# Optimization experiments

Hardware: AMD Instinct MI355X
Metric: run time of the kernel (lower is better)

## Reference

```python
import jax, jax.numpy as jnp
import numpy as np

H = 16      # num_heads
EPS = 1e-6  # LayerNorm eps


def _ln(x, g, b):
    m = jnp.mean(x, -1, keepdims=True)
    v = jnp.mean((x - m) ** 2, -1, keepdims=True)
    return (x - m) / jnp.sqrt(v + EPS) * g + b


def _mha(q_in, k_in, v_in, qw, qb, kw, kb, vw, vb, pw, pb, mask):
    # q_in: (B, Sq, C); k_in/v_in: (B, Skv, C); mask: bool (Sq, Skv) or None (True = masked)
    B, Sq, C = q_in.shape
    hd = C // H

    def split(x, w, bb):
        return (x @ w + bb).reshape(B, -1, H, hd).transpose(0, 2, 1, 3)  # (B,H,S,hd)

    q = split(q_in, qw, qb) * hd ** -0.5
    k = split(k_in, kw, kb)
    v = split(v_in, vw, vb)
    s = jnp.einsum('bhqd,bhkd->bhqk', q, k)  # (B,H,Sq,Skv)
    if mask is not None:
        s = jnp.where(mask, -jnp.inf, s)
    a = jax.nn.softmax(s, axis=-1)
    o = jnp.einsum('bhqk,bhkd->bhqd', a, v)
    return o.transpose(0, 2, 1, 3).reshape(B, Sq, C) @ pw + pb


def _mlp(x, w1, b1, w2, b2):
    # torch nn.GELU default is exact (erf) gelu
    return jax.nn.gelu(x @ w1 + b1, approximate=False) @ w2 + b2


def setup_inputs() -> dict:
    key = jax.random.key(0)
    B, S, C, M = 1, 2048, 1024, 4096
    ks = iter(jax.random.split(key, 64))

    def w(shape):
        return jax.random.normal(next(ks), shape, jnp.float32) * 0.02

    inp = {
        'features': jax.random.normal(next(ks), (B, S, C), jnp.float32),
        'encoder_output': jax.random.normal(next(ks), (B, S, C), jnp.float32),
    }
    for p in ['ln1a', 'ln1b', 'ln2a', 'ln2b']:
        inp[p + '_g'] = jnp.ones((C,), jnp.float32)
        inp[p + '_b'] = jnp.zeros((C,), jnp.float32)
    for p in ['sa', 'ca']:
        for q in ['q', 'k', 'v', 'p']:
            inp[f'{p}_{q}w'] = w((C, C))
            inp[f'{p}_{q}b'] = jnp.zeros((C,), jnp.float32)
    for p in ['m1', 'm2']:
        inp[p + '_w1'] = w((C, M))
        inp[p + '_b1'] = jnp.zeros((M,), jnp.float32)
        inp[p + '_w2'] = w((M, C))
        inp[p + '_b2'] = jnp.zeros((C,), jnp.float32)
    return inp


def reference(features, encoder_output,
              ln1a_g, ln1a_b, ln1b_g, ln1b_b, ln2a_g, ln2a_b, ln2b_g, ln2b_b,
              sa_qw, sa_qb, sa_kw, sa_kb, sa_vw, sa_vb, sa_pw, sa_pb,
              ca_qw, ca_qb, ca_kw, ca_kb, ca_vw, ca_vb, ca_pw, ca_pb,
              m1_w1, m1_b1, m1_w2, m1_b2, m2_w1, m2_b1, m2_w2, m2_b2):
    S = features.shape[1]
    causal = jnp.triu(jnp.ones((S, S), dtype=bool), 1)  # look-ahead mask (decoder)
    # self-attention block (pre-norm, residual; dropout/drop-path identity in eval)
    xn = _ln(features, ln1a_g, ln1a_b)
    x = features + _mha(xn, xn, xn, sa_qw, sa_qb, sa_kw, sa_kb, sa_vw, sa_vb, sa_pw, sa_pb, causal)
    x = x + _mlp(_ln(x, ln1b_g, ln1b_b), m1_w1, m1_b1, m1_w2, m1_b2)
    # cross-attention block: k = v = encoder_output, q = norm(x)
    xn = _ln(x, ln2a_g, ln2a_b)
    x = x + _mha(xn, encoder_output, encoder_output, ca_qw, ca_qb, ca_kw, ca_kb, ca_vw, ca_vb, ca_pw, ca_pb, None)
    return x + _mlp(_ln(x, ln2b_g, ln2b_b), m2_w1, m2_b1, m2_w2, m2_b2)
```

## Files before the change

### kernel.cpp

```cpp
#include <hip/hip_runtime.h>
#include <math.h>

typedef unsigned short u16;
typedef __bf16 bf16_t;
typedef bf16_t bf16x8 __attribute__((ext_vector_type(8)));
typedef float f32x4 __attribute__((ext_vector_type(4)));
typedef float f32x16 __attribute__((ext_vector_type(16)));

#define DI __device__ __forceinline__

DI u16 f2bf(float f) {
  union { float f; unsigned u; } c; c.f = f;
  unsigned r = c.u + 0x7FFFu + ((c.u >> 16) & 1u);
  return (u16)(r >> 16);
}

DI unsigned pack2(float lo, float hi_) {
  return (unsigned)f2bf(lo) | ((unsigned)f2bf(hi_) << 16);
}

typedef __attribute__((address_space(1))) void* gas_ptr;
typedef __attribute__((address_space(3))) void* las_ptr;

DI void gload16(const void* g, void* l) {
  __builtin_amdgcn_global_load_lds((gas_ptr)g, (las_ptr)l, 16, 0, 0);
}

struct TransArgs { const float* src[12]; u16* dst[12]; };
__global__ __launch_bounds__(256) void k_transpose_all(TransArgs ta) {
  __shared__ float tile[32][33];
  int bx = blockIdx.x;
  int z, local, K, N;
  if (bx < 8192) { z = bx >> 10; local = bx & 1023; K = 1024; N = 1024; }
  else {
    int i = bx - 8192; z = 8 + (i >> 12); local = i & 4095;
    if (z & 1) { K = 4096; N = 1024; } else { K = 1024; N = 4096; }
  }
  const float* w = ta.src[z];
  u16* wt = ta.dst[z];
  int nT = N >> 5;
  int n0 = (local % nT) * 32, k0 = (local / nT) * 32;
  int tx = threadIdx.x & 31, ty = threadIdx.x >> 5;
  for (int r = ty; r < 32; r += 8)
    tile[r][tx] = w[(size_t)(k0 + r) * N + n0 + tx];
  __syncthreads();
  for (int r = ty; r < 32; r += 8)
    wt[(size_t)(n0 + r) * K + k0 + tx] = f2bf(tile[tx][r]);
}

__global__ __launch_bounds__(256) void k_cvt(const float* __restrict__ in, u16* __restrict__ out, int n4) {
  int i = blockIdx.x * 256 + threadIdx.x;
  if (i < n4) {
    float4 v = ((const float4*)in)[i];
    ushort4 o;
    o.x = f2bf(v.x); o.y = f2bf(v.y); o.z = f2bf(v.z); o.w = f2bf(v.w);
    ((ushort4*)out)[i] = o;
  }
}

__global__ __launch_bounds__(256) void k_biaspack(float* __restrict__ bq, float* __restrict__ bc,
                                                  const float* qb, const float* kb, const float* vb,
                                                  const float* ckb, const float* cvb) {
  int i = blockIdx.x * 256 + threadIdx.x;
  if (i < 1024) bq[i] = qb[i];
  else if (i < 2048) bq[i] = kb[i - 1024];
  else if (i < 3072) bq[i] = vb[i - 2048];
  else if (i < 4096) bc[i - 3072] = ckb[i - 3072];
  else if (i < 5120) bc[i - 3072] = cvb[i - 4096];
}

__global__ __launch_bounds__(256) void k_ln(const float* __restrict__ x, const float* __restrict__ g,
                                            const float* __restrict__ b, u16* __restrict__ out) {
  int row = blockIdx.x, t = threadIdx.x;
  const float4 v = ((const float4*)(x + (size_t)row * 1024))[t];
  float s = v.x + v.y + v.z + v.w;
  float ss = v.x * v.x + v.y * v.y + v.z * v.z + v.w * v.w;
  for (int o = 32; o; o >>= 1) { s += __shfl_down(s, o); ss += __shfl_down(ss, o); }
  __shared__ float red[10];
  int w = t >> 6;
  if ((t & 63) == 0) { red[w] = s; red[4 + w] = ss; }
  __syncthreads();
  if (t == 0) {
    float S = red[0] + red[1] + red[2] + red[3];
    float SS = red[4] + red[5] + red[6] + red[7];
    float mean = S * (1.f / 1024.f);
    float var = SS * (1.f / 1024.f) - mean * mean;
    red[8] = mean; red[9] = rsqrtf(var + 1e-6f);
  }
  __syncthreads();
  float mean = red[8], rstd = red[9];
  float4 gg = ((const float4*)g)[t], bb = ((const float4*)b)[t];
  ushort4 o4;
  o4.x = f2bf((v.x - mean) * rstd * gg.x + bb.x);
  o4.y = f2bf((v.y - mean) * rstd * gg.y + bb.y);
  o4.z = f2bf((v.z - mean) * rstd * gg.z + bb.z);
  o4.w = f2bf((v.w - mean) * rstd * gg.w + bb.w);
  ((ushort4*)(out + (size_t)row * 1024))[t] = o4;
}

template <int MODE>
__global__ __launch_bounds__(256) void k_gemm(const u16* __restrict__ A, const u16* __restrict__ Bt,
                                              const float* __restrict__ bias, void* outv, u16* vtout,
                                              int M, int N, int K, int ostride,
                                              float scale, int scale_end, int vcol0) {
  constexpr int BM = 64, NT = 2;
  __shared__ u16 aL[2][BM * 64];
  __shared__ u16 bL[2][128 * 64];
  const int lane = threadIdx.x & 63, w = threadIdx.x >> 6, t = threadIdx.x;
  const int wn = w;
  const int m0 = blockIdx.y * BM, n0 = blockIdx.x * 128;

  f32x4 acc[4][NT];
#pragma unroll
  for (int i = 0; i < 4; ++i)
#pragma unroll
    for (int j = 0; j < NT; ++j) acc[i][j] = (f32x4){0.f, 0.f, 0.f, 0.f};

  auto stage = [&](int buf, int kt) {
    const int k0 = kt << 6;
#pragma unroll
    for (int c = t; c < BM * 8; c += 256) {
      int row = c >> 3, c16 = c & 7;
      int sw = (c16 * 16) ^ ((row & 7) << 4);
      gload16((const char*)(A + (size_t)(m0 + row) * K + k0) + sw, (char*)aL[buf] + c * 16);
    }
#pragma unroll
    for (int c = t; c < 1024; c += 256) {
      int row = c >> 3, c16 = c & 7;
      int sw = (c16 * 16) ^ ((row & 7) << 4);
      gload16((const char*)(Bt + (size_t)(n0 + row) * K + k0) + sw, (char*)bL[buf] + c * 16);
    }
  };

  const int nkt = K >> 6;
  stage(0, 0);
  __syncthreads();
  int cur = 0;
  for (int kt = 0; kt < nkt; ++kt) {
    if (kt + 1 < nkt) stage(cur ^ 1, kt + 1);
#pragma unroll
    for (int kk = 0; kk < 2; ++kk) {
      const int cb = kk * 64 + ((lane >> 4) << 4);
      bf16x8 af[4], bfr[NT];
#pragma unroll
      for (int mi = 0; mi < 4; ++mi) {
        int row = mi * 16 + (lane & 15);
        af[mi] = *(const bf16x8*)((const char*)aL[cur] + row * 128 + (cb ^ ((row & 7) << 4)));
      }
#pragma unroll
      for (int ni = 0; ni < NT; ++ni) {
        int row = wn * 32 + ni * 16 + (lane & 15);
        bfr[ni] = *(const bf16x8*)((const char*)bL[cur] + row * 128 + (cb ^ ((row & 7) << 4)));
      }
#pragma unroll
      for (int mi = 0; mi < 4; ++mi)
#pragma unroll
        for (int ni = 0; ni < NT; ++ni)
          acc[mi][ni] = __builtin_amdgcn_mfma_f32_16x16x32_bf16(af[mi], bfr[ni], acc[mi][ni], 0, 0, 0);
    }
    __syncthreads();
    cur ^= 1;
  }

  const int cBase = n0 + wn * 32 + (lane & 15);
  const int rBase = m0 + ((lane >> 4) << 2);
#pragma unroll
  for (int ni = 0; ni < NT; ++ni) {
    int col = cBase + ni * 16;
    float bv = bias[col];
#pragma unroll
    for (int mi = 0; mi < 4; ++mi) {
      int row = rBase + mi * 16;
      f32x4 a = acc[mi][ni];
      if (MODE == 0) {
        float sc = (col < scale_end) ? scale : 1.f;
        if (col >= vcol0) {
          ushort4 o4;
          o4.x = f2bf((a[0] + bv) * sc); o4.y = f2bf((a[1] + bv) * sc);
          o4.z = f2bf((a[2] + bv) * sc); o4.w = f2bf((a[3] + bv) * sc);
          *(ushort4*)(vtout + (size_t)(col - vcol0) * M + row) = o4;
        } else {
#pragma unroll
          for (int r = 0; r < 4; ++r)
            ((u16*)outv)[(size_t)(row + r) * ostride + col] = f2bf((a[r] + bv) * sc);
        }
      } else {
#pragma unroll
        for (int r = 0; r < 4; ++r) {
          float v = a[r] + bv;
          ((u16*)outv)[(size_t)(row + r) * ostride + col] =
              f2bf(0.5f * v * (1.f + erff(v * 0.70710678118654752f)));
        }
      }
    }
  }
}

template <int MODE>
__global__ __launch_bounds__(512, 2) void k_gemm_sk(const u16* __restrict__ A, const u16* __restrict__ Bt,
                                                    const float* __restrict__ bias, const float* res,
                                                    void* outv, int M, int N, int K, float scale) {
  __shared__ u16 aL[2][2][64 * 64];
  __shared__ u16 bL[2][2][64 * 64];
  const int t = threadIdx.x, lane = t & 63, w = t >> 6;
  const int kh = w >> 2, ws2 = w & 3;
  const int ts = t & 255;
  const int m0 = blockIdx.y * 64, n0 = blockIdx.x * 64;
  const int nktH = (K >> 6) >> 1;
  const int kbase = kh * nktH;

  f32x4 acc[4];
#pragma unroll
  for (int i = 0; i < 4; ++i) acc[i] = (f32x4){0.f, 0.f, 0.f, 0.f};

  auto stage = [&](int buf, int kt) {
    const int k0 = (kbase + kt) << 6;
#pragma unroll
    for (int i = 0; i < 2; ++i) {
      int c = i * 256 + ts;
      int row = c >> 3, c16 = c & 7;
      int sw = (c16 * 16) ^ ((row & 7) << 4);
      gload16((const char*)(A + (size_t)(m0 + row) * K + k0) + sw, (char*)aL[kh][buf] + c * 16);
      gload16((const char*)(Bt + (size_t)(n0 + row) * K + k0) + sw, (char*)bL[kh][buf] + c * 16);
    }
  };

  stage(0, 0);
  __syncthreads();
  int cur = 0;
  for (int kt = 0; kt < nktH; ++kt) {
    if (kt + 1 < nktH) stage(cur ^ 1, kt + 1);
#pragma unroll
    for (int kk = 0; kk < 2; ++kk) {
      const int cb = kk * 64 + ((lane >> 4) << 4);
      bf16x8 af[4], bfr;
#pragma unroll
      for (int mi = 0; mi < 4; ++mi) {
        int row = mi * 16 + (lane & 15);
        af[mi] = *(const bf16x8*)((const char*)aL[kh][cur] + row * 128 + (cb ^ ((row & 7) << 4)));
      }
      {
        int row = ws2 * 16 + (lane & 15);
        bfr = *(const bf16x8*)((const char*)bL[kh][cur] + row * 128 + (cb ^ ((row & 7) << 4)));
      }
#pragma unroll
      for (int mi = 0; mi < 4; ++mi)
        acc[mi] = __builtin_amdgcn_mfma_f32_16x16x32_bf16(af[mi], bfr, acc[mi], 0, 0, 0);
    }
    __syncthreads();
    cur ^= 1;
  }

  float* mergeF = (float*)aL;
  const int r0l = (lane >> 4) << 2, col16 = lane & 15;
  if (kh == 1) {
#pragma unroll
    for (int mi = 0; mi < 4; ++mi)
#pragma unroll
      for (int r = 0; r < 4; ++r)
        mergeF[(ws2 * 64 + mi * 16 + r0l + r) * 17 + col16] = acc[mi][r];
  }
  __syncthreads();
  if (kh == 0) {
    int col = n0 + ws2 * 16 + col16;
    float bv = bias[col];
#pragma unroll
    for (int mi = 0; mi < 4; ++mi) {
      int row = m0 + mi * 16 + r0l;
#pragma unroll
      for (int r = 0; r < 4; ++r) {
        float v = acc[mi][r] + mergeF[(ws2 * 64 + mi * 16 + r0l + r) * 17 + col16] + bv;
        size_t idx = (size_t)(row + r) * N + col;
        if (MODE == 0) ((u16*)outv)[idx] = f2bf(v * scale);
        else ((float*)outv)[idx] = res[idx] + v;
      }
    }
  }
}

template <bool CAUSAL>
__global__ __launch_bounds__(512, 2) void k_attn3(const u16* __restrict__ Q, const u16* __restrict__ K,
                                                  const u16* __restrict__ VT, u16* __restrict__ O,
                                                  int S, int qstride, int kstride) {
  __shared__ __align__(16) char smem[64 * 1024 + 2048 + 8192];
  const int t = threadIdx.x, lane = t & 63, w = t >> 6;
  const int ks = w & 3, qw = w >> 2;
  const int lo5 = lane & 31, hi = lane >> 5;
  const int h = blockIdx.x;
  const int bq = blockIdx.y;
  const int qt = (bq & 1) ? (31 - (bq >> 1)) : (bq >> 1);
  const int hd0 = h * 64;
  const int q0 = qt * 64 + qw * 32;
  const int ts = qw * 64 + lane;

  u16* kL = (u16*)(smem + ks * 16384);
  u16* vL = (u16*)(smem + ks * 16384 + 8192);

  bf16x8 qf[4];
#pragma unroll
  for (int sl = 0; sl < 4; ++sl)
    qf[sl] = *(const bf16x8*)(Q + (size_t)(q0 + lo5) * qstride + hd0 + sl * 16 + hi * 8);

  f32x16 oa0 = {}, oa1 = {};
  float mrun = -1e30f, lsum = 0.f;

  const int nkt = CAUSAL ? (qt + 1) : (S >> 6);
  const int nIter = (nkt + 3) >> 2;

  for (int i = 0; i < nIter; ++i) {
    const int kt = ks + 4 * i;
    const bool active = kt < nkt;
    if (active) {
#pragma unroll
      for (int j = 0; j < 4; ++j) {
        int c = j * 128 + ts, row = c >> 3, c16 = c & 7;
        int sw = (c16 * 16) ^ ((row & 7) << 4);
        gload16((const char*)(K + (size_t)(kt * 64 + row) * kstride + hd0) + sw, (char*)kL + c * 16);
      }
#pragma unroll
      for (int j = 0; j < 4; ++j) {
        int c = j * 128 + ts, row = c >> 3, c16 = c & 7;
        int sw = (c16 * 16) ^ ((row & 7) << 4);
        gload16((const char*)(VT + (size_t)(hd0 + row) * S + kt * 64) + sw, (char*)vL + c * 16);
      }
    }
    __syncthreads();
    if (active) {
      f32x16 s0 = {}, s1 = {};
#pragma unroll
      for (int sl = 0; sl < 4; ++sl) {
        int cb = sl * 32 + hi * 16;
        int r0 = lo5, r1 = 32 + lo5;
        bf16x8 kf0 = *(const bf16x8*)((const char*)kL + r0 * 128 + (cb ^ ((r0 & 7) << 4)));
        bf16x8 kf1 = *(const bf16x8*)((const char*)kL + r1 * 128 + (cb ^ ((r1 & 7) << 4)));
        s0 = __builtin_amdgcn_mfma_f32_32x32x16_bf16(kf0, qf[sl], s0, 0, 0, 0);
        s1 = __builtin_amdgcn_mfma_f32_32x32x16_bf16(kf1, qf[sl], s1, 0, 0, 0);
      }

      if (CAUSAL && kt == qt) {
        int qg = q0 + lo5;
#pragma unroll
        for (int r = 0; r < 16; ++r) {
          int kg = kt * 64 + (r & 3) + 8 * (r >> 2) + 4 * hi;
          if (kg > qg) s0[r] = -1e30f;
          if (kg + 32 > qg) s1[r] = -1e30f;
        }
      }

      float pm = s0[0];
#pragma unroll
      for (int r = 1; r < 16; ++r) pm = fmaxf(pm, s0[r]);
#pragma unroll
      for (int r = 0; r < 16; ++r) pm = fmaxf(pm, s1[r]);
      pm = fmaxf(pm, __shfl_xor(pm, 32));

      float mnew = fmaxf(mrun, pm);
      float sc = exp2f(mrun - mnew);
      lsum *= sc;
#pragma unroll
      for (int r = 0; r < 16; ++r) { oa0[r] *= sc; oa1[r] *= sc; }
      mrun = mnew;

      float ps = 0.f;
#pragma unroll
      for (int r = 0; r < 16; ++r) { s0[r] = exp2f(s0[r] - mrun); ps += s0[r]; }
#pragma unroll
      for (int r = 0; r < 16; ++r) { s1[r] = exp2f(s1[r] - mrun); ps += s1[r]; }
      ps += __shfl_xor(ps, 32);
      lsum += ps;

#pragma unroll
      for (int ksl = 0; ksl < 4; ++ksl) {
        const int base = 8 * (ksl & 1);
        float pA0, pA1, pA2, pA3, pB0, pB1, pB2, pB3;
        if (ksl < 2) {
          pA0 = s0[base + 0]; pA1 = s0[base + 1]; pA2 = s0[base + 2]; pA3 = s0[base + 3];
          pB0 = s0[base + 4]; pB1 = s0[base + 5]; pB2 = s0[base + 6]; pB3 = s0[base + 7];
        } else {
          pA0 = s1[base + 0]; pA1 = s1[base + 1]; pA2 = s1[base + 2]; pA3 = s1[base + 3];
          pB0 = s1[base + 4]; pB1 = s1[base + 5]; pB2 = s1[base + 6]; pB3 = s1[base + 7];
        }
        unsigned a01 = pack2(pA0, pA1), a23 = pack2(pA2, pA3);
        unsigned b01 = pack2(pB0, pB1), b23 = pack2(pB2, pB3);
        unsigned xa01 = __shfl_xor(a01, 32), xa23 = __shfl_xor(a23, 32);
        unsigned xb01 = __shfl_xor(b01, 32), xb23 = __shfl_xor(b23, 32);
        union { unsigned u[4]; bf16x8 v; } pf;
        pf.u[0] = hi ? xb01 : a01;
        pf.u[1] = hi ? xb23 : a23;
        pf.u[2] = hi ? b01 : xa01;
        pf.u[3] = hi ? b23 : xa23;
        int cb = ksl * 32 + hi * 16;
        int r0 = lo5, r1 = 32 + lo5;
        bf16x8 vf0 = *(const bf16x8*)((const char*)vL + r0 * 128 + (cb ^ ((r0 & 7) << 4)));
        bf16x8 vf1 = *(const bf16x8*)((const char*)vL + r1 * 128 + (cb ^ ((r1 & 7) << 4)));
        oa0 = __builtin_amdgcn_mfma_f32_32x32x16_bf16(vf0, pf.v, oa0, 0, 0, 0);
        oa1 = __builtin_amdgcn_mfma_f32_32x32x16_bf16(vf1, pf.v, oa1, 0, 0, 0);
      }
    }
    __syncthreads();
  }

  float* mlBuf = (float*)(smem + 65536);
#define OB_BYTE(g, halfoff) (lo5 * 256 + (((halfoff) + 32 * (g) + 16 * hi) ^ ((lo5 & 15) << 4)))
  if (ks >= 2) {
    char* ob = smem + (qw * 2 + (ks - 2)) * 8192;
#pragma unroll
    for (int g = 0; g < 4; ++g) {
      *(float4*)(ob + OB_BYTE(g, 0)) = make_float4(oa0[4 * g + 0], oa0[4 * g + 1], oa0[4 * g + 2], oa0[4 * g + 3]);
      *(float4*)(ob + OB_BYTE(g, 128)) = make_float4(oa1[4 * g + 0], oa1[4 * g + 1], oa1[4 * g + 2], oa1[4 * g + 3]);
    }
    if (hi == 0) { mlBuf[(w * 32 + lo5) * 2] = mrun; mlBuf[(w * 32 + lo5) * 2 + 1] = lsum; }
  }
  __syncthreads();
  if (ks < 2) {
    int pw = qw * 4 + ks + 2;
    char* ob = smem + (qw * 2 + ks) * 8192;
    float mB = mlBuf[(pw * 32 + lo5) * 2], lB = mlBuf[(pw * 32 + lo5) * 2 + 1];
    float M = fmaxf(mrun, mB);
    float sA = exp2f(mrun - M), sB = exp2f(mB - M);
    lsum = lsum * sA + lB * sB;
    mrun = M;
#pragma unroll
    for (int g = 0; g < 4; ++g) {
      float4 v0 = *(const float4*)(ob + OB_BYTE(g, 0));
      float4 v1 = *(const float4*)(ob + OB_BYTE(g, 128));
      oa0[4 * g + 0] = oa0[4 * g + 0] * sA + v0.x * sB;
      oa0[4 * g + 1] = oa0[4 * g + 1] * sA + v0.y * sB;
      oa0[4 * g + 2] = oa0[4 * g + 2] * sA + v0.z * sB;
      oa0[4 * g + 3] = oa0[4 * g + 3] * sA + v0.w * sB;
      oa1[4 * g + 0] = oa1[4 * g + 0] * sA + v1.x * sB;
      oa1[4 * g + 1] = oa1[4 * g + 1] * sA + v1.y * sB;
      oa1[4 * g + 2] = oa1[4 * g + 2] * sA + v1.z * sB;
      oa1[4 * g + 3] = oa1[4 * g + 3] * sA + v1.w * sB;
    }
  }
  if (ks == 1) {
    char* ob = smem + 32768 + qw * 8192;
#pragma unroll
    for (int g = 0; g < 4; ++g) {
      *(float4*)(ob + OB_BYTE(g, 0)) = make_float4(oa0[4 * g + 0], oa0[4 * g + 1], oa0[4 * g + 2], oa0[4 * g + 3]);
      *(float4*)(ob + OB_BYTE(g, 128)) = make_float4(oa1[4 * g + 0], oa1[4 * g + 1], oa1[4 * g + 2], oa1[4 * g + 3]);
    }
    if (hi == 0) { mlBuf[(w * 32 + lo5) * 2] = mrun; mlBuf[(w * 32 + lo5) * 2 + 1] = lsum; }
  }
  __syncthreads();
  if (ks == 0) {
    int pw = qw * 4 + 1;
    char* ob = smem + 32768 + qw * 8192;
    float mB = mlBuf[(pw * 32 + lo5) * 2], lB = mlBuf[(pw * 32 + lo5) * 2 + 1];
    float M = fmaxf(mrun, mB);
    float sA = exp2f(mrun - M), sB = exp2f(mB - M);
    lsum = lsum * sA + lB * sB;
#pragma unroll
    for (int g = 0; g < 4; ++g) {
      float4 v0 = *(const float4*)(ob + OB_BYTE(g, 0));
      float4 v1 = *(const float4*)(ob + OB_BYTE(g, 128));
      oa0[4 * g + 0] = oa0[4 * g + 0] * sA + v0.x * sB;
      oa0[4 * g + 1] = oa0[4 * g + 1] * sA + v0.y * sB;
      oa0[4 * g + 2] = oa0[4 * g + 2] * sA + v0.z * sB;
      oa0[4 * g + 3] = oa0[4 * g + 3] * sA + v0.w * sB;
      oa1[4 * g + 0] = oa1[4 * g + 0] * sA + v1.x * sB;
      oa1[4 * g + 1] = oa1[4 * g + 1] * sA + v1.y * sB;
      oa1[4 * g + 2] = oa1[4 * g + 2] * sA + v1.z * sB;
      oa1[4 * g + 3] = oa1[4 * g + 3] * sA + v1.w * sB;
    }
    float inv = 1.f / lsum;
    u16* ldsO = (u16*)(smem + 65536 + 2048);
    int qrow = qw * 32 + lo5;
#pragma unroll
    for (int g = 0; g < 4; ++g) {
      unsigned w0 = pack2(oa0[4 * g + 0] * inv, oa0[4 * g + 1] * inv);
      unsigned w1 = pack2(oa0[4 * g + 2] * inv, oa0[4 * g + 3] * inv);
      int dby = (8 * g + 4 * hi) * 2;
      *(uint2*)((char*)ldsO + qrow * 128 + (dby ^ ((qrow & 7) << 4))) = make_uint2(w0, w1);
      unsigned w2 = pack2(oa1[4 * g + 0] * inv, oa1[4 * g + 1] * inv);
      unsigned w3 = pack2(oa1[4 * g + 2] * inv, oa1[4 * g + 3] * inv);
      int dby2 = (32 + 8 * g + 4 * hi) * 2;
      *(uint2*)((char*)ldsO + qrow * 128 + (dby2 ^ ((qrow & 7) << 4))) = make_uint2(w2, w3);
    }
  }
  __syncthreads();
  {
    u16* ldsO = (u16*)(smem + 65536 + 2048);
    int c = t, row = c >> 3, c16 = c & 7;
    uint4 val = *(const uint4*)((const char*)ldsO + row * 128 + ((c16 * 16) ^ ((row & 7) << 4)));
    *(uint4*)(O + (size_t)(qt * 64 + row) * 1024 + hd0 + c16 * 8) = val;
  }
#undef OB_BYTE
}

extern "C" void kernel_launch(void* const* d_in, const int* in_sizes, int n_in,
                              void* d_out, int out_size, void* d_ws, size_t ws_size,
                              hipStream_t stream) {
  const float* features = (const float*)d_in[0];
  const float* enc      = (const float*)d_in[1];
  const float* g1a = (const float*)d_in[2];  const float* b1a = (const float*)d_in[3];
  const float* g1b = (const float*)d_in[4];  const float* b1b = (const float*)d_in[5];
  const float* g2a = (const float*)d_in[6];  const float* b2a = (const float*)d_in[7];
  const float* g2b = (const float*)d_in[8];  const float* b2b = (const float*)d_in[9];
  const float* sa_qw = (const float*)d_in[10]; const float* sa_qb = (const float*)d_in[11];
  const float* sa_kw = (const float*)d_in[12]; const float* sa_kb = (const float*)d_in[13];
  const float* sa_vw = (const float*)d_in[14]; const float* sa_vb = (const float*)d_in[15];
  const float* sa_pw = (const float*)d_in[16]; const float* sa_pb = (const float*)d_in[17];
  const float* ca_qw = (const float*)d_in[18]; const float* ca_qb = (const float*)d_in[19];
  const float* ca_kw = (const float*)d_in[20]; const float* ca_kb = (const float*)d_in[21];
  const float* ca_vw = (const float*)d_in[22]; const float* ca_vb = (const float*)d_in[23];
  const float* ca_pw = (const float*)d_in[24]; const float* ca_pb = (const float*)d_in[25];
  const float* m1_w1 = (const float*)d_in[26]; const float* m1_b1 = (const float*)d_in[27];
  const float* m1_w2 = (const float*)d_in[28]; const float* m1_b2 = (const float*)d_in[29];
  const float* m2_w1 = (const float*)d_in[30]; const float* m2_b1 = (const float*)d_in[31];
  const float* m2_w2 = (const float*)d_in[32]; const float* m2_b2 = (const float*)d_in[33];

  const int S = 2048, C = 1024, Mh = 4096;
  const size_t CC = (size_t)C * C;
  float* xout = (float*)d_out;

  char* p = (char*)d_ws;
  auto take = [&](size_t bytes) { char* q = p; p += (bytes + 255) & ~(size_t)255; return q; };
  u16* wt_qkv  = (u16*)take(3 * CC * 2);
  u16* wt_sap  = (u16*)take(CC * 2);
  u16* wt_cap  = (u16*)take(CC * 2);
  u16* wt_caq  = (u16*)take(CC * 2);
  u16* wt_ckv  = (u16*)take(2 * CC * 2);
  u16* wt_m1w1 = (u16*)take((size_t)C * Mh * 2);
  u16* wt_m1w2 = (u16*)take((size_t)C * Mh * 2);
  u16* wt_m2w1 = (u16*)take((size_t)C * Mh * 2);
  u16* wt_m2w2 = (u16*)take((size_t)C * Mh * 2);
  float* bias_qkv = (float*)take(3 * C * 4);
  float* bias_ckv = (float*)take(2 * C * 4);
  u16* xn   = (u16*)take((size_t)S * C * 2);
  u16* encb = (u16*)take((size_t)S * C * 2);
  u16* vtbuf = (u16*)take((size_t)C * S * 2);
  u16* abuf  = (u16*)take((size_t)S * C * 2);
  u16* hbuf  = (u16*)take((size_t)S * Mh * 2);
  u16* qkbuf = hbuf;
  u16* qbuf  = hbuf + (size_t)4 * 1024 * 1024;
  u16* kvbuf = hbuf + (size_t)6 * 1024 * 1024;

  dim3 blk(256);
  const float qs2 = 0.125f * 1.4426950408889634f;
  const int BIG = 1 << 30;

  TransArgs ta;
  ta.src[0] = sa_qw;  ta.dst[0] = wt_qkv;
  ta.src[1] = sa_kw;  ta.dst[1] = wt_qkv + CC;
  ta.src[2] = sa_vw;  ta.dst[2] = wt_qkv + 2 * CC;
  ta.src[3] = sa_pw;  ta.dst[3] = wt_sap;
  ta.src[4] = ca_pw;  ta.dst[4] = wt_cap;
  ta.src[5] = ca_qw;  ta.dst[5] = wt_caq;
  ta.src[6] = ca_kw;  ta.dst[6] = wt_ckv;
  ta.src[7] = ca_vw;  ta.dst[7] = wt_ckv + CC;
  ta.src[8] = m1_w1;  ta.dst[8] = wt_m1w1;
  ta.src[9] = m1_w2;  ta.dst[9] = wt_m1w2;
  ta.src[10] = m2_w1; ta.dst[10] = wt_m2w1;
  ta.src[11] = m2_w2; ta.dst[11] = wt_m2w2;
  k_transpose_all<<<dim3(8192 + 16384), blk, 0, stream>>>(ta);
  k_cvt<<<dim3(S * C / 1024), blk, 0, stream>>>(enc, encb, S * C / 4);
  k_biaspack<<<20, blk, 0, stream>>>(bias_qkv, bias_ckv, sa_qb, sa_kb, sa_vb, ca_kb, ca_vb);

  k_ln<<<S, blk, 0, stream>>>(features, g1a, b1a, xn);
  k_gemm<0><<<dim3(24, 32), blk, 0, stream>>>(xn, wt_qkv, bias_qkv, qkbuf, vtbuf,
                                              S, 3072, C, 2048, qs2, 1024, 2048);
  k_attn3<true><<<dim3(16, 32), dim3(512), 0, stream>>>(qkbuf, qkbuf + 1024, vtbuf, abuf, S, 2048, 2048);
  k_gemm_sk<1><<<dim3(16, 32), dim3(512), 0, stream>>>(abuf, wt_sap, sa_pb, features, xout, S, C, C, 1.f);
  k_ln<<<S, blk, 0, stream>>>(xout, g1b, b1b, xn);
  k_gemm<2><<<dim3(32, 32), blk, 0, stream>>>(xn, wt_m1w1, m1_b1, hbuf, nullptr,
                                              S, Mh, C, Mh, 1.f, 0, BIG);
  k_gemm_sk<1><<<dim3(16, 32), dim3(512), 0, stream>>>(hbuf, wt_m1w2, m1_b2, xout, xout, S, C, Mh, 1.f);
  k_ln<<<S, blk, 0, stream>>>(xout, g2a, b2a, xn);
  k_gemm_sk<0><<<dim3(16, 32), dim3(512), 0, stream>>>(xn, wt_caq, ca_qb, nullptr, qbuf, S, C, C, qs2);
  k_gemm<0><<<dim3(16, 32), blk, 0, stream>>>(encb, wt_ckv, bias_ckv, kvbuf, vtbuf,
                                              S, 2048, C, 1024, 1.f, 0, 1024);
  k_attn3<false><<<dim3(16, 32), dim3(512), 0, stream>>>(qbuf, kvbuf, vtbuf, abuf, S, 1024, 1024);
  k_gemm_sk<1><<<dim3(16, 32), dim3(512), 0, stream>>>(abuf, wt_cap, ca_pb, xout, xout, S, C, C, 1.f);
  k_ln<<<S, blk, 0, stream>>>(xout, g2b, b2b, xn);
  k_gemm<2><<<dim3(32, 32), blk, 0, stream>>>(xn, wt_m2w1, m2_b1, hbuf, nullptr,
                                              S, Mh, C, Mh, 1.f, 0, BIG);
  k_gemm_sk<1><<<dim3(16, 32), dim3(512), 0, stream>>>(hbuf, wt_m2w2, m2_b2, xout, xout, S, C, Mh, 1.f);
}
```

Baseline: 371.2 us.

## Prefetch next K/V tiles during attention compute and add lazy softmax rescale

```diff
diff --git a/kernel.cpp b/kernel.cpp
--- a/kernel.cpp
+++ b/kernel.cpp
@@ -17,6 +17,12 @@
 
 DI unsigned pack2(float lo, float hi_) {
   return (unsigned)f2bf(lo) | ((unsigned)f2bf(hi_) << 16);
+}
+
+DI unsigned cvt_pk(float lo, float hi_) {
+  unsigned d;
+  asm("v_cvt_pk_bf16_f32 %0, %1, %2" : "=v"(d) : "v"(lo), "v"(hi_));
+  return d;
 }
 
 typedef __attribute__((address_space(1))) void* gas_ptr;
@@ -296,6 +302,23 @@
   u16* kL = (u16*)(smem + ks * 16384);
   u16* vL = (u16*)(smem + ks * 16384 + 8192);
 
+  auto issueK = [&](int kt) {
+#pragma unroll
+    for (int j = 0; j < 4; ++j) {
+      int c = j * 128 + ts, row = c >> 3, c16 = c & 7;
+      int sw = (c16 * 16) ^ ((row & 7) << 4);
+      gload16((const char*)(K + (size_t)(kt * 64 + row) * kstride + hd0) + sw, (char*)kL + c * 16);
+    }
+  };
+  auto issueV = [&](int kt) {
+#pragma unroll
+    for (int j = 0; j < 4; ++j) {
+      int c = j * 128 + ts, row = c >> 3, c16 = c & 7;
+      int sw = (c16 * 16) ^ ((row & 7) << 4);
+      gload16((const char*)(VT + (size_t)(hd0 + row) * S + kt * 64) + sw, (char*)vL + c * 16);
+    }
+  };
+
   bf16x8 qf[4];
 #pragma unroll
   for (int sl = 0; sl < 4; ++sl)
@@ -306,27 +329,16 @@
 
   const int nkt = CAUSAL ? (qt + 1) : (S >> 6);
   const int nIter = (nkt + 3) >> 2;
+
+  if (ks < nkt) { issueK(ks); issueV(ks); }
+  __syncthreads();
 
   for (int i = 0; i < nIter; ++i) {
     const int kt = ks + 4 * i;
     const bool active = kt < nkt;
+    const bool nxt = kt + 4 < nkt;
+    f32x16 s0 = {}, s1 = {};
     if (active) {
-#pragma unroll
-      for (int j = 0; j < 4; ++j) {
-        int c = j * 128 + ts, row = c >> 3, c16 = c & 7;
-        int sw = (c16 * 16) ^ ((row & 7) << 4);
-        gload16((const char*)(K + (size_t)(kt * 64 + row) * kstride + hd0) + sw, (char*)kL + c * 16);
-      }
-#pragma unroll
-      for (int j = 0; j < 4; ++j) {
-        int c = j * 128 + ts, row = c >> 3, c16 = c & 7;
-        int sw = (c16 * 16) ^ ((row & 7) << 4);
-        gload16((const char*)(VT + (size_t)(hd0 + row) * S + kt * 64) + sw, (char*)vL + c * 16);
-      }
-    }
-    __syncthreads();
-    if (active) {
-      f32x16 s0 = {}, s1 = {};
 #pragma unroll
       for (int sl = 0; sl < 4; ++sl) {
         int cb = sl * 32 + hi * 16;
@@ -336,7 +348,6 @@
         s0 = __builtin_amdgcn_mfma_f32_32x32x16_bf16(kf0, qf[sl], s0, 0, 0, 0);
         s1 = __builtin_amdgcn_mfma_f32_32x32x16_bf16(kf1, qf[sl], s1, 0, 0, 0);
       }
-
       if (CAUSAL && kt == qt) {
         int qg = q0 + lo5;
 #pragma unroll
@@ -346,29 +357,42 @@
           if (kg + 32 > qg) s1[r] = -1e30f;
         }
       }
-
-      float pm = s0[0];
-#pragma unroll
-      for (int r = 1; r < 16; ++r) pm = fmaxf(pm, s0[r]);
-#pragma unroll
-      for (int r = 0; r < 16; ++r) pm = fmaxf(pm, s1[r]);
-      pm = fmaxf(pm, __shfl_xor(pm, 32));
-
-      float mnew = fmaxf(mrun, pm);
-      float sc = exp2f(mrun - mnew);
-      lsum *= sc;
-#pragma unroll
-      for (int r = 0; r < 16; ++r) { oa0[r] *= sc; oa1[r] *= sc; }
-      mrun = mnew;
-
-      float ps = 0.f;
-#pragma unroll
-      for (int r = 0; r < 16; ++r) { s0[r] = exp2f(s0[r] - mrun); ps += s0[r]; }
-#pragma unroll
-      for (int r = 0; r < 16; ++r) { s1[r] = exp2f(s1[r] - mrun); ps += s1[r]; }
-      ps += __shfl_xor(ps, 32);
-      lsum += ps;
-
+      float mx[16];
+#pragma unroll
+      for (int r = 0; r < 16; ++r) mx[r] = fmaxf(s0[r], s1[r]);
+#pragma unroll
+      for (int st = 8; st; st >>= 1)
+#pragma unroll
+        for (int r = 0; r < 8; ++r)
+          if (r < st) mx[r] = fmaxf(mx[r], mx[r + st]);
+      float pm = fmaxf(mx[0], __shfl_xor(mx[0], 32));
+
+      if (!__all(pm - mrun <= 8.f)) {
+        float mnew = fmaxf(mrun, pm);
+        float sc = exp2f(mrun - mnew);
+        lsum *= sc;
+#pragma unroll
+        for (int r = 0; r < 16; ++r) { oa0[r] *= sc; oa1[r] *= sc; }
+        mrun = mnew;
+      }
+
+#pragma unroll
+      for (int r = 0; r < 16; ++r) s0[r] = exp2f(s0[r] - mrun);
+#pragma unroll
+      for (int r = 0; r < 16; ++r) s1[r] = exp2f(s1[r] - mrun);
+      float sm[16];
+#pragma unroll
+      for (int r = 0; r < 16; ++r) sm[r] = s0[r] + s1[r];
+#pragma unroll
+      for (int st = 8; st; st >>= 1)
+#pragma unroll
+        for (int r = 0; r < 8; ++r)
+          if (r < st) sm[r] += sm[r + st];
+      lsum += sm[0] + __shfl_xor(sm[0], 32);
+    }
+    __syncthreads();
+    if (nxt) issueK(kt + 4);
+    if (active) {
 #pragma unroll
       for (int ksl = 0; ksl < 4; ++ksl) {
         const int base = 8 * (ksl & 1);
@@ -380,8 +404,8 @@
           pA0 = s1[base + 0]; pA1 = s1[base + 1]; pA2 = s1[base + 2]; pA3 = s1[base + 3];
           pB0 = s1[base + 4]; pB1 = s1[base + 5]; pB2 = s1[base + 6]; pB3 = s1[base + 7];
         }
-        unsigned a01 = pack2(pA0, pA1), a23 = pack2(pA2, pA3);
-        unsigned b01 = pack2(pB0, pB1), b23 = pack2(pB2, pB3);
+        unsigned a01 = cvt_pk(pA0, pA1), a23 = cvt_pk(pA2, pA3);
+        unsigned b01 = cvt_pk(pB0, pB1), b23 = cvt_pk(pB2, pB3);
         unsigned xa01 = __shfl_xor(a01, 32), xa23 = __shfl_xor(a23, 32);
         unsigned xb01 = __shfl_xor(b01, 32), xb23 = __shfl_xor(b23, 32);
         union { unsigned u[4]; bf16x8 v; } pf;
@@ -398,7 +422,9 @@
       }
     }
     __syncthreads();
-  }
+    if (nxt) issueV(kt + 4);
+  }
+  __syncthreads();
 
   float* mlBuf = (float*)(smem + 65536);
 #define OB_BYTE(g, halfoff) (lo5 * 256 + (((halfoff) + 32 * (g) + 16 * hi) ^ ((lo5 & 15) << 4)))
@@ -469,12 +495,12 @@
     int qrow = qw * 32 + lo5;
 #pragma unroll
     for (int g = 0; g < 4; ++g) {
-      unsigned w0 = pack2(oa0[4 * g + 0] * inv, oa0[4 * g + 1] * inv);
-      unsigned w1 = pack2(oa0[4 * g + 2] * inv, oa0[4 * g + 3] * inv);
+      unsigned w0 = cvt_pk(oa0[4 * g + 0] * inv, oa0[4 * g + 1] * inv);
+      unsigned w1 = cvt_pk(oa0[4 * g + 2] * inv, oa0[4 * g + 3] * inv);
       int dby = (8 * g + 4 * hi) * 2;
       *(uint2*)((char*)ldsO + qrow * 128 + (dby ^ ((qrow & 7) << 4))) = make_uint2(w0, w1);
-      unsigned w2 = pack2(oa1[4 * g + 0] * inv, oa1[4 * g + 1] * inv);
-      unsigned w3 = pack2(oa1[4 * g + 2] * inv, oa1[4 * g + 3] * inv);
+      unsigned w2 = cvt_pk(oa1[4 * g + 0] * inv, oa1[4 * g + 1] * inv);
+      unsigned w3 = cvt_pk(oa1[4 * g + 2] * inv, oa1[4 * g + 3] * inv);
       int dby2 = (32 + 8 * g + 4 * hi) * 2;
       *(uint2*)((char*)ldsO + qrow * 128 + (dby2 ^ ((qrow & 7) << 4))) = make_uint2(w2, w3);
     }
```

After: 360.4 us. 2.9% less time.
